# Kernel tuning notes

Hardware: AMD Instinct MI355X
Metric: run time of the kernel (lower is better)

Reference implementation:

```python
import jax, jax.numpy as jnp
import numpy as np
from jax import lax


def binarize(x):
    # tf.sign with 0 mapped to +1
    return jnp.where(x >= 0, jnp.ones_like(x), -jnp.ones_like(x))


def setup_inputs() -> dict:
    key = jax.random.key(0)
    kx, kw = jax.random.split(key)
    x = jax.random.normal(kx, (64, 56, 56, 128), dtype=jnp.float32)
    # weights init: normal stddev=0.1, shape (kh, kw, in_ch, filters) == HWIO
    w = jax.random.normal(kw, (3, 3, 128, 256), dtype=jnp.float32) * 0.1
    return {"x": x, "w": w}


def reference(x, w):
    x_bin = binarize(x)
    w_bin = binarize(w)
    # NHWC input, HWIO kernel, SAME padding, stride (1,1)
    out = lax.conv_general_dilated(
        x_bin, w_bin,
        window_strides=(1, 1),
        padding="SAME",
        dimension_numbers=("NHWC", "HWIO", "NHWC"),
    )
    return out
```

## Files before the change

kernel.cpp:

```cpp
#include <hip/hip_runtime.h>
#include <stdint.h>


#define IH 56
#define IW 56
#define CIN 128
#define COUT 256
#define NBATCH 64

__global__ void pack_x_kernel(const float* __restrict__ x,
                              uint64_t* __restrict__ xp, int npix) {
    int gtid = blockIdx.x * blockDim.x + threadIdx.x;
    int wave = gtid >> 6;
    int lane = gtid & 63;
    int nwaves = (gridDim.x * blockDim.x) >> 6;
    for (int p = wave; p < npix; p += nwaves) {
        float a = x[(size_t)p * CIN + lane];
        float b = x[(size_t)p * CIN + 64 + lane];
        uint64_t m0 = __ballot(a < 0.0f);
        uint64_t m1 = __ballot(b < 0.0f);
        if (lane == 0) {
            xp[2 * (size_t)p]     = m0;
            xp[2 * (size_t)p + 1] = m1;
        }
    }
}

__global__ void pack_w_kernel(const float* __restrict__ w,
                              uint64_t* __restrict__ wp) {
    int gtid = blockIdx.x * blockDim.x + threadIdx.x;
    int wave = gtid >> 6;
    int lane = gtid & 63;
    int nwaves = (gridDim.x * blockDim.x) >> 6;
    const int ntask = COUT * 9;
    for (int t = wave; t < ntask; t += nwaves) {
        int oc  = t / 9;
        int tap = t % 9;
        float a = w[((size_t)tap * CIN + lane) * COUT + oc];
        float b = w[((size_t)tap * CIN + 64 + lane) * COUT + oc];
        uint64_t m0 = __ballot(a < 0.0f);
        uint64_t m1 = __ballot(b < 0.0f);
        if (lane == 0) {
            wp[2 * (size_t)t]     = m0;
            wp[2 * (size_t)t + 1] = m1;
        }
    }
}

__global__ __launch_bounds__(256) void bconv_kernel(
        const uint64_t* __restrict__ xp,
        const uint64_t* __restrict__ wp,
        float* __restrict__ out) {
    __shared__ alignas(16) uint64_t xs[3][IW][2];

    int nh = blockIdx.x;
    int h  = nh % IH;
    int n  = nh / IH;
    int oc = threadIdx.x;

    for (int i = threadIdx.x; i < 3 * IW; i += blockDim.x) {
        int kh = i / IW, c = i % IW;
        int r = h - 1 + kh;
        if ((unsigned)r < IH) {
            size_t p = ((size_t)n * IH + r) * IW + c;
            xs[kh][c][0] = xp[2 * p];
            xs[kh][c][1] = xp[2 * p + 1];
        }
    }

    uint64_t wr[18];
#pragma unroll
    for (int t = 0; t < 9; ++t) {
        wr[2 * t]     = wp[((size_t)oc * 9 + t) * 2];
        wr[2 * t + 1] = wp[((size_t)oc * 9 + t) * 2 + 1];
    }
    __syncthreads();

    size_t obase = (size_t)nh * IW * COUT + oc;
    for (int w = 0; w < IW; ++w) {
        int popc = 0, valid = 0;
#pragma unroll
        for (int kh = 0; kh < 3; ++kh) {
            int r = h - 1 + kh;
            if ((unsigned)r >= IH) continue;
#pragma unroll
            for (int kw = 0; kw < 3; ++kw) {
                int c = w - 1 + kw;
                if ((unsigned)c >= IW) continue;
                valid++;
                int t = kh * 3 + kw;
                popc += __popcll(xs[kh][c][0] ^ wr[2 * t])
                      + __popcll(xs[kh][c][1] ^ wr[2 * t + 1]);
            }
        }
        out[obase + (size_t)w * COUT] = (float)(valid * CIN - 2 * popc);
    }
}

extern "C" void kernel_launch(void* const* d_in, const int* in_sizes, int n_in,
                              void* d_out, int out_size, void* d_ws, size_t ws_size,
                              hipStream_t stream) {
    const float* x = (const float*)d_in[0];
    const float* w = (const float*)d_in[1];
    float* out = (float*)d_out;

    uint64_t* wp = (uint64_t*)d_ws;
    uint64_t* xp = (uint64_t*)((char*)d_ws + (64 << 10));

    const int npix = NBATCH * IH * IW;

    pack_x_kernel<<<2048, 256, 0, stream>>>(x, xp, npix);
    pack_w_kernel<<<144, 256, 0, stream>>>(w, wp);
    bconv_kernel<<<NBATCH * IH, 256, 0, stream>>>(xp, wp, out);
}
```

Baseline: 376.2 us.

## Fuse input binarization into conv kernel and process two rows per block

```diff
diff --git a/kernel.cpp b/kernel.cpp
--- a/kernel.cpp
+++ b/kernel.cpp
@@ -6,95 +6,124 @@
 #define IW 56
 #define CIN 128
 #define COUT 256
-#define NBATCH 64
-
-__global__ void pack_x_kernel(const float* __restrict__ x,
-                              uint64_t* __restrict__ xp, int npix) {
-    int gtid = blockIdx.x * blockDim.x + threadIdx.x;
-    int wave = gtid >> 6;
-    int lane = gtid & 63;
-    int nwaves = (gridDim.x * blockDim.x) >> 6;
-    for (int p = wave; p < npix; p += nwaves) {
-        float a = x[(size_t)p * CIN + lane];
-        float b = x[(size_t)p * CIN + 64 + lane];
-        uint64_t m0 = __ballot(a < 0.0f);
-        uint64_t m1 = __ballot(b < 0.0f);
-        if (lane == 0) {
-            xp[2 * (size_t)p]     = m0;
-            xp[2 * (size_t)p + 1] = m1;
-        }
-    }
-}
+#define NB 64
 
 __global__ void pack_w_kernel(const float* __restrict__ w,
                               uint64_t* __restrict__ wp) {
     int gtid = blockIdx.x * blockDim.x + threadIdx.x;
-    int wave = gtid >> 6;
-    int lane = gtid & 63;
-    int nwaves = (gridDim.x * blockDim.x) >> 6;
-    const int ntask = COUT * 9;
-    for (int t = wave; t < ntask; t += nwaves) {
-        int oc  = t / 9;
-        int tap = t % 9;
-        float a = w[((size_t)tap * CIN + lane) * COUT + oc];
-        float b = w[((size_t)tap * CIN + 64 + lane) * COUT + oc];
-        uint64_t m0 = __ballot(a < 0.0f);
-        uint64_t m1 = __ballot(b < 0.0f);
-        if (lane == 0) {
-            wp[2 * (size_t)t]     = m0;
-            wp[2 * (size_t)t + 1] = m1;
-        }
+    int wave = gtid >> 6, lane = gtid & 63;
+    int nw = (gridDim.x * blockDim.x) >> 6;
+    const int ntask = 9 * 2 * COUT;
+    for (int t = wave; t < ntask; t += nw) {
+        int oc = t & 255, hf = (t >> 8) & 1, tap = t >> 9;
+        float v = w[((size_t)(tap * CIN + hf * 64 + lane)) * COUT + oc];
+        uint64_t m = __ballot(v < 0.0f);
+        if (lane == 0) wp[(size_t)(tap * 2 + hf) * COUT + oc] = m;
     }
 }
 
-__global__ __launch_bounds__(256) void bconv_kernel(
-        const uint64_t* __restrict__ xp,
+__device__ __forceinline__ int popc9(const uint64_t X[3][2], const uint64_t Y[3][2],
+                                     const uint64_t Z[3][2], const uint64_t wr[9][2]) {
+    int s = 0;
+#pragma unroll
+    for (int kh = 0; kh < 3; ++kh) {
+        s += __popcll(X[kh][0] ^ wr[kh * 3 + 0][0]) + __popcll(X[kh][1] ^ wr[kh * 3 + 0][1]);
+        s += __popcll(Y[kh][0] ^ wr[kh * 3 + 1][0]) + __popcll(Y[kh][1] ^ wr[kh * 3 + 1][1]);
+        s += __popcll(Z[kh][0] ^ wr[kh * 3 + 2][0]) + __popcll(Z[kh][1] ^ wr[kh * 3 + 2][1]);
+    }
+    return s;
+}
+
+#define LOADCOL(dst, rb, cc)                                    \
+    do {                                                        \
+        _Pragma("unroll")                                       \
+        for (int _k = 0; _k < 3; ++_k) {                        \
+            dst[_k][0] = xs[(rb) + _k][(cc)][0];                \
+            dst[_k][1] = xs[(rb) + _k][(cc)][1];                \
+        }                                                       \
+    } while (0)
+
+__global__ __launch_bounds__(256, 4) void bconv_kernel(
+        const float* __restrict__ x,
         const uint64_t* __restrict__ wp,
         float* __restrict__ out) {
-    __shared__ alignas(16) uint64_t xs[3][IW][2];
+    __shared__ alignas(16) uint64_t xs[4][58][2];
 
-    int nh = blockIdx.x;
-    int h  = nh % IH;
-    int n  = nh / IH;
-    int oc = threadIdx.x;
+    int bh = blockIdx.x % 28;
+    int n  = blockIdx.x / 28;
+    int h0 = bh * 2;
+    int tid = threadIdx.x, oc = tid;
+    int wv = tid >> 6, lane = tid & 63;
 
-    for (int i = threadIdx.x; i < 3 * IW; i += blockDim.x) {
-        int kh = i / IW, c = i % IW;
-        int r = h - 1 + kh;
-        if ((unsigned)r < IH) {
-            size_t p = ((size_t)n * IH + r) * IW + c;
-            xs[kh][c][0] = xp[2 * p];
-            xs[kh][c][1] = xp[2 * p + 1];
-        }
+    uint64_t wr[9][2];
+#pragma unroll
+    for (int t = 0; t < 9; ++t) {
+        wr[t][0] = wp[(size_t)(t * 2 + 0) * COUT + oc];
+        wr[t][1] = wp[(size_t)(t * 2 + 1) * COUT + oc];
     }
 
-    uint64_t wr[18];
-#pragma unroll
-    for (int t = 0; t < 9; ++t) {
-        wr[2 * t]     = wp[((size_t)oc * 9 + t) * 2];
-        wr[2 * t + 1] = wp[((size_t)oc * 9 + t) * 2 + 1];
+    uint64_t* xf = &xs[0][0][0];
+    for (int i = tid; i < 4 * 58 * 2; i += 256) xf[i] = 0;
+    __syncthreads();
+
+    for (int task = wv; task < 4 * IW; task += 4) {
+        int kh = task / IW, col = task % IW;
+        int r = h0 - 1 + kh;
+        if ((unsigned)r < IH) {
+            const float* px = x + (((size_t)n * IH + r) * IW + col) * CIN;
+            float a = px[lane];
+            float b = px[64 + lane];
+            uint64_t m0 = __ballot(a < 0.0f);
+            uint64_t m1 = __ballot(b < 0.0f);
+            if (lane == 0) { xs[kh][col + 1][0] = m0; xs[kh][col + 1][1] = m1; }
+        }
     }
     __syncthreads();
 
-    size_t obase = (size_t)nh * IW * COUT + oc;
-    for (int w = 0; w < IW; ++w) {
-        int popc = 0, valid = 0;
+    int pcw[9];
 #pragma unroll
-        for (int kh = 0; kh < 3; ++kh) {
-            int r = h - 1 + kh;
-            if ((unsigned)r >= IH) continue;
-#pragma unroll
-            for (int kw = 0; kw < 3; ++kw) {
-                int c = w - 1 + kw;
-                if ((unsigned)c >= IW) continue;
-                valid++;
-                int t = kh * 3 + kw;
-                popc += __popcll(xs[kh][c][0] ^ wr[2 * t])
-                      + __popcll(xs[kh][c][1] ^ wr[2 * t + 1]);
-            }
+    for (int t = 0; t < 9; ++t) pcw[t] = __popcll(wr[t][0]) + __popcll(wr[t][1]);
+    int rs0 = pcw[0] + pcw[1] + pcw[2];
+    int rs2 = pcw[6] + pcw[7] + pcw[8];
+    int cs0 = pcw[0] + pcw[3] + pcw[6];
+    int cs2 = pcw[2] + pcw[5] + pcw[8];
+
+    bool eA = (h0 == 0);
+    int vhA = eA ? 2 : 3, invA = eA ? rs0 : 0;
+    int c0A = eA ? pcw[0] : 0, c2A = eA ? pcw[2] : 0;
+    int KintA = 384 * vhA + 2 * invA;
+    int K0A = 256 * vhA + 2 * (invA + cs0 - c0A);
+    int K55A = 256 * vhA + 2 * (invA + cs2 - c2A);
+
+    bool eB = (h0 + 1 == IH - 1);
+    int vhB = eB ? 2 : 3, invB = eB ? rs2 : 0;
+    int c0B = eB ? pcw[6] : 0, c2B = eB ? pcw[8] : 0;
+    int KintB = 384 * vhB + 2 * invB;
+    int K0B = 256 * vhB + 2 * (invB + cs0 - c0B);
+    int K55B = 256 * vhB + 2 * (invB + cs2 - c2B);
+
+    auto conv_row = [&](int rb, int K0, int Kint, int K55, float* po) {
+        uint64_t A[3][2], B[3][2], C[3][2];
+        LOADCOL(A, rb, 0);
+        LOADCOL(B, rb, 1);
+        LOADCOL(C, rb, 2);
+        po[0] = (float)(K0 - 2 * popc9(A, B, C, wr)); po += COUT;
+        LOADCOL(A, rb, 3);
+        po[0] = (float)(Kint - 2 * popc9(B, C, A, wr)); po += COUT;
+        for (int wb = 2; wb <= 53; wb += 3) {
+            LOADCOL(B, rb, wb + 2);
+            po[0] = (float)(Kint - 2 * popc9(C, A, B, wr)); po += COUT;
+            LOADCOL(C, rb, wb + 3);
+            po[0] = (float)(Kint - 2 * popc9(A, B, C, wr)); po += COUT;
+            LOADCOL(A, rb, wb + 4);
+            int k = (wb == 53) ? K55 : Kint;
+            po[0] = (float)(k - 2 * popc9(B, C, A, wr)); po += COUT;
         }
-        out[obase + (size_t)w * COUT] = (float)(valid * CIN - 2 * popc);
-    }
+    };
+
+    float* poA = out + (((size_t)n * IH + h0) * IW) * COUT + oc;
+    conv_row(0, K0A, KintA, K55A, poA);
+    conv_row(1, K0B, KintB, K55B, poA + (size_t)IW * COUT);
 }
 
 extern "C" void kernel_launch(void* const* d_in, const int* in_sizes, int n_in,
@@ -103,13 +132,8 @@
     const float* x = (const float*)d_in[0];
     const float* w = (const float*)d_in[1];
     float* out = (float*)d_out;
+    uint64_t* wp = (uint64_t*)d_ws;
 
-    uint64_t* wp = (uint64_t*)d_ws;
-    uint64_t* xp = (uint64_t*)((char*)d_ws + (64 << 10));
-
-    const int npix = NBATCH * IH * IW;
-
-    pack_x_kernel<<<2048, 256, 0, stream>>>(x, xp, npix);
-    pack_w_kernel<<<144, 256, 0, stream>>>(w, wp);
-    bconv_kernel<<<NBATCH * IH, 256, 0, stream>>>(xp, wp, out);
+    pack_w_kernel<<<288, 256, 0, stream>>>(w, wp);
+    bconv_kernel<<<NB * 28, 256, 0, stream>>>(x, wp, out);
 }
```

Measured after the change: 389.6 us. 1.04x slower.
